# Performance work log

Hardware: AMD Instinct MI355X
Metric: run time of the kernel (lower is better)

The kernel has to match this reference:

```python
import jax, jax.numpy as jnp
import numpy as np

B, S, D = 4, 2048, 512
H, DK, DV = 8, 64, 64

def setup_inputs() -> dict:
    key = jax.random.key(0)
    ks = jax.random.split(key, 11)
    s = 0.02
    return {
        "q_in": jax.random.normal(ks[0], (B, S, D), jnp.float32),
        "k_in": jax.random.normal(ks[1], (B, S, D), jnp.float32),
        "v_in": jax.random.normal(ks[2], (B, S, D), jnp.float32),
        "Wq": jax.random.normal(ks[3], (H, D, DK), jnp.float32) * s,
        "bq": jax.random.normal(ks[4], (H, DK), jnp.float32) * s,
        "Wk": jax.random.normal(ks[5], (H, D, DK), jnp.float32) * s,
        "bk": jax.random.normal(ks[6], (H, DK), jnp.float32) * s,
        "Wv": jax.random.normal(ks[7], (H, D, DV), jnp.float32) * s,
        "bv": jax.random.normal(ks[8], (H, DV), jnp.float32) * s,
        "Wo": jax.random.normal(ks[9], (H * DV, D), jnp.float32) * s,
        "bo": jax.random.normal(ks[10], (D,), jnp.float32) * s,
    }


def reference(q_in, k_in, v_in, Wq, bq, Wk, bk, Wv, bv, Wo, bo):
    # Per-head Q/K/V projections, batched over heads (same math as the
    # original Python loop over SingleAttention heads).
    q = jnp.einsum("bsd,hdk->bhsk", q_in, Wq) + bq[None, :, None, :]   # [B,H,S,DK]
    k = jnp.einsum("bsd,hdk->bhsk", k_in, Wk) + bk[None, :, None, :]   # [B,H,S,DK]
    v = jnp.einsum("bsd,hdv->bhsv", v_in, Wv) + bv[None, :, None, :]   # [B,H,S,DV]
    scale = 1.0 / jnp.sqrt(jnp.float32(DK))
    scores = jnp.einsum("bhqk,bhsk->bhqs", q, k) * scale               # [B,H,S,S]
    attn = jax.nn.softmax(scores, axis=-1)
    out = jnp.einsum("bhqs,bhsv->bhqv", attn, v)                        # [B,H,S,DV]
    # concat heads along feature dim: [B,S,H*DV]
    concat = out.transpose(0, 2, 1, 3).reshape(B, S, H * DV)
    return concat @ Wo + bo                                             # [B,S,D]
```

## Files before the change

### kernel.cpp

```cpp
#include <hip/hip_runtime.h>
#include <hip/hip_bf16.h>

using bf16 = __hip_bfloat16;
typedef short short8  __attribute__((ext_vector_type(8)));
typedef short short4v __attribute__((ext_vector_type(4)));
typedef float float4v __attribute__((ext_vector_type(4)));
typedef float f32x16  __attribute__((ext_vector_type(16)));
typedef unsigned int uint4v __attribute__((ext_vector_type(4)));

#define MFMA_BF16   __builtin_amdgcn_mfma_f32_16x16x32_bf16
#define MFMA32_BF16 __builtin_amdgcn_mfma_f32_32x32x16_bf16

#define B_  4
#define S_  2048
#define D_  512
#define H_  8
#define DK_ 64

__device__ __forceinline__ short f2bf(float f) {
  bf16 h = __float2bfloat16(f);
  return *reinterpret_cast<short*>(&h);
}

__device__ __forceinline__ unsigned cvtpk(float lo, float hi) {
  unsigned r;
  asm("v_cvt_pk_bf16_f32 %0, %1, %2" : "=v"(r) : "v"(lo), "v"(hi));
  return r;
}

__device__ __forceinline__ void plswap(unsigned& a, unsigned& b) {
  asm("v_permlane32_swap_b32 %0, %1" : "+v"(a), "+v"(b));
}

__device__ __forceinline__ short8 mk8(unsigned v0, unsigned v1, unsigned v2,
                                      unsigned v3) {
  uint4v u;
  u[0] = v0; u[1] = v1; u[2] = v2; u[3] = v3;
  return __builtin_bit_cast(short8, u);
}

#define GLL(g, l) __builtin_amdgcn_global_load_lds(                        \
      (const __attribute__((address_space(1))) void*)(g),                  \
      (__attribute__((address_space(3))) void*)(l), 16, 0, 0)

__global__ __launch_bounds__(256)
void prep(const float* __restrict__ qin, const float* __restrict__ kin,
          const float* __restrict__ vin, short* __restrict__ Xb,
          const float* __restrict__ Wq, const float* __restrict__ Wk,
          const float* __restrict__ Wv, const float* __restrict__ Wo,
          short* __restrict__ WqT, short* __restrict__ WkT,
          short* __restrict__ WvT, short* __restrict__ WoT) {
  __shared__ float tile[64 * 65];
  const int bid = blockIdx.x, tid = threadIdx.x;
  const size_t NTOK = (size_t)B_ * S_ * D_;

  if (bid < 6144) {
    const int z = bid >> 11, blk = bid & 2047;
    const float* src = (z == 0) ? qin : (z == 1) ? kin : vin;
    short* dst = Xb + (size_t)z * NTOK;
    const size_t base = ((size_t)blk * 256 + tid) * 8;
    float4v f0 = *(const float4v*)&src[base];
    float4v f1 = *(const float4v*)&src[base + 4];
    short8 s;
#pragma unroll
    for (int j = 0; j < 4; j++) { s[j] = f2bf(f0[j]); s[j + 4] = f2bf(f1[j]); }
    *(short8*)&dst[base] = s;
    return;
  }

  const int tw = bid - 6144;
  const int mat = tw >> 6, t = tw & 63;
  const float* W = (mat == 0) ? Wq : (mat == 1) ? Wk : (mat == 2) ? Wv : Wo;
  short* T       = (mat == 0) ? WqT : (mat == 1) ? WkT : (mat == 2) ? WvT : WoT;

  size_t sbase, ss, dbase;
  if (mat < 3) {
    int hh = t >> 3, d0 = (t & 7) * 64;
    sbase = (size_t)hh * 32768 + (size_t)d0 * 64;
    ss = 64;
    dbase = (size_t)hh * 64 * 512 + d0;
  } else {
    int n0 = (t >> 3) * 64, k0 = (t & 7) * 64;
    sbase = (size_t)k0 * 512 + n0;
    ss = 512;
    dbase = (size_t)n0 * 512 + k0;
  }

  {
    int r = tid >> 2, c0 = (tid & 3) * 16;
#pragma unroll
    for (int j = 0; j < 4; j++)
      *(float4v*)&tile[r * 65 + c0 + j * 4] =
          *(const float4v*)&W[sbase + (size_t)r * ss + c0 + j * 4];
  }
  __syncthreads();
  {
    int c = tid >> 2, r0 = (tid & 3) * 16;
#pragma unroll
    for (int j = 0; j < 2; j++) {
      short8 s;
#pragma unroll
      for (int u = 0; u < 8; u++) s[u] = f2bf(tile[(r0 + j * 8 + u) * 65 + c]);
      *(short8*)&T[dbase + (size_t)c * 512 + r0 + j * 8] = s;
    }
  }
}

__device__ __forceinline__ void gemm_core2(const short* __restrict__ A,
                                           const short* __restrict__ Bt,
                                           int m0, int n0,
                                           short* As, short* Bs,
                                           float4v acc[4][4]) {
  const int tid  = threadIdx.x;
  const int lane = tid & 63, wave = tid >> 6;
  const int quad = lane >> 4, l16 = lane & 15;
  const int wm = (wave >> 1) * 64, wn = (wave & 1) * 64;

  auto stage = [&](int buf, int k0) {
#pragma unroll
    for (int i = 0; i < 4; i++) {
      int sl = wave * 256 + i * 64 + lane;
      int row = sl >> 3, cs = sl & 7;
      int gc = (cs ^ (row & 7)) << 3;
      GLL(&A[(size_t)(m0 + row) * 512 + k0 + gc],
          &As[buf * 8192 + (wave * 256 + i * 64) * 8]);
      GLL(&Bt[(size_t)(n0 + row) * 512 + k0 + gc],
          &Bs[buf * 8192 + (wave * 256 + i * 64) * 8]);
    }
  };
  auto comp = [&](int buf) {
#pragma unroll
    for (int ks = 0; ks < 64; ks += 32) {
      const int sr = (ks >> 3) + quad;
      short8 af[4], bfr[4];
#pragma unroll
      for (int mi = 0; mi < 4; mi++) {
        int row = wm + mi * 16 + l16;
        af[mi] = *(short8*)&As[buf * 8192 + row * 64 + ((sr ^ (row & 7)) << 3)];
      }
#pragma unroll
      for (int ni = 0; ni < 4; ni++) {
        int row = wn + ni * 16 + l16;
        bfr[ni] = *(short8*)&Bs[buf * 8192 + row * 64 + ((sr ^ (row & 7)) << 3)];
      }
#pragma unroll
      for (int mi = 0; mi < 4; mi++)
#pragma unroll
        for (int ni = 0; ni < 4; ni++)
          acc[mi][ni] = MFMA_BF16(af[mi], bfr[ni], acc[mi][ni], 0, 0, 0);
    }
  };

  stage(0, 0);
  asm volatile("s_waitcnt vmcnt(0)" ::: "memory");
  __syncthreads();
#pragma unroll
  for (int k0 = 0; k0 < 512; k0 += 128) {
    stage(1, k0 + 64);
    comp(0);
    asm volatile("s_waitcnt vmcnt(0)" ::: "memory");
    __syncthreads();
    if (k0 + 128 < 512) stage(0, k0 + 128);
    comp(1);
    asm volatile("s_waitcnt vmcnt(0)" ::: "memory");
    __syncthreads();
  }
}

__global__ __launch_bounds__(256, 2)
void qkv_gemm(const short* __restrict__ Xb,
              const short* __restrict__ WqT, const short* __restrict__ WkT,
              const short* __restrict__ WvT,
              const float* __restrict__ bq, const float* __restrict__ bk,
              const float* __restrict__ bv,
              short* __restrict__ Qp, short* __restrict__ Kp,
              short* __restrict__ Vt) {
  __shared__ __align__(16) short As[2 * 128 * 64];
  __shared__ __align__(16) short Bs[2 * 128 * 64];
  const int m0 = blockIdx.x * 128, n0 = blockIdx.y * 128;
  const int z = blockIdx.z;
  const size_t NTOK = (size_t)B_ * S_ * D_;
  const short* A    = Xb + (size_t)z * NTOK;
  const short* Bt   = (z == 0) ? WqT : (z == 1) ? WkT : WvT;
  const float* bias = (z == 0) ? bq  : (z == 1) ? bk  : bv;
  const float scale = (z == 0) ? 0.125f * 1.44269504088896f : 1.0f;

  float4v acc[4][4];
#pragma unroll
  for (int mi = 0; mi < 4; mi++)
#pragma unroll
    for (int ni = 0; ni < 4; ni++) acc[mi][ni] = (float4v){0.f, 0.f, 0.f, 0.f};

  gemm_core2(A, Bt, m0, n0, As, Bs, acc);

  const int lane = threadIdx.x & 63, wave = threadIdx.x >> 6;
  const int quad = lane >> 4, l16 = lane & 15;
  const int wm = (wave >> 1) * 64, wn = (wave & 1) * 64;

  if (z < 2) {
    short* out = (z == 0) ? Qp : Kp;
#pragma unroll
    for (int mi = 0; mi < 4; mi++) {
      int m = m0 + wm + mi * 16 + quad * 4;
      int b = m >> 11, s = m & 2047;
#pragma unroll
      for (int ni = 0; ni < 4; ni++) {
        int n = n0 + wn + ni * 16 + l16;
        int h = n >> 6, dk = n & 63;
        float bb = bias[n];
        size_t base = (((size_t)b * H_ + h) * S_ + s) * 64 + dk;
#pragma unroll
        for (int r = 0; r < 4; r++)
          out[base + (size_t)r * 64] = f2bf((acc[mi][ni][r] + bb) * scale);
      }
    }
  } else {
#pragma unroll
    for (int mi = 0; mi < 4; mi++) {
      int m = m0 + wm + mi * 16 + quad * 4;
      int b = m >> 11, s = m & 2047;
#pragma unroll
      for (int ni = 0; ni < 4; ni++) {
        int n = n0 + wn + ni * 16 + l16;
        int h = n >> 6, v = n & 63;
        float bb = bias[n];
        short4v pk;
#pragma unroll
        for (int r = 0; r < 4; r++) pk[r] = f2bf(acc[mi][ni][r] + bb);
        *(short4v*)&Vt[(((size_t)b * H_ + h) * 64 + v) * S_ + s] = pk;
      }
    }
  }
}

__global__ __launch_bounds__(512, 4)
void attn_kernel(const short* __restrict__ Qp, const short* __restrict__ Kp,
                 const short* __restrict__ Vt, short* __restrict__ Ao) {
  __shared__ __align__(16) short sh[32768];

  const int orig = blockIdx.y * gridDim.x + blockIdx.x;
  const int lb = (orig & 7) * 64 + (orig >> 3);
  const int qt = lb & 15, bh = lb >> 4;
  const int b = bh >> 3, h = bh & 7;

  const int tid = threadIdx.x;
  const int lane = tid & 63, wave = tid >> 6;
  const int wg = wave & 3, half = wave >> 2;
  const int l31 = lane & 31, hi = lane >> 5, s7 = l31 & 7;

  const short* Qb = Qp + (size_t)bh * S_ * 64;
  const short* Kb = Kp + (size_t)bh * S_ * 64 + (size_t)half * 1024 * 64;
  const short* Vb = Vt + (size_t)bh * 64 * S_;

  short8 qf[4];
  {
    const short* qrow = Qb + (size_t)(qt * 128 + wg * 32 + l31) * 64;
#pragma unroll
    for (int w = 0; w < 4; w++)
      qf[w] = *(const short8*)&qrow[w * 16 + hi * 8];
  }

  const int slot0 = wg * 128 + lane;
  const int kr0 = slot0 >> 3, kc0 = slot0 & 7;
  const int kr1 = kr0 + 8;
  const short* kg0 = Kb + (size_t)kr0 * 64 + ((kc0 ^ (kr0 & 7)) << 3);
  const short* kg1 = Kb + (size_t)kr1 * 64 + ((kc0 ^ (kr1 & 7)) << 3);
  const short* vg0 = Vb + (size_t)kr0 * S_ + half * 1024 + ((kc0 ^ (kr0 & 7)) << 3);
  const short* vg1 = Vb + (size_t)kr1 * S_ + half * 1024 + ((kc0 ^ (kr1 & 7)) << 3);

  short* Kbase = sh;
  short* Vbase = sh + 16384;

  f32x16 acc0, acc1;
#pragma unroll
  for (int r = 0; r < 16; r++) { acc0[r] = 0.f; acc1[r] = 0.f; }
  float ls0 = 0.f, ls1 = 0.f;

  {
    short* kd = Kbase + (half * 2) * 4096 + wg * 1024;
    short* vd = Vbase + (half * 2) * 4096 + wg * 1024;
    GLL(kg0, kd); GLL(kg1, kd + 512);
    GLL(vg0, vd); GLL(vg1, vd + 512);
  }
  __syncthreads();

  for (int t = 0; t < 16; t++) {
    const int cur = t & 1;
    if (t < 15) {
      short* kd = Kbase + (half * 2 + (cur ^ 1)) * 4096 + wg * 1024;
      short* vd = Vbase + (half * 2 + (cur ^ 1)) * 4096 + wg * 1024;
      GLL(kg0 + (size_t)(t + 1) * 4096, kd);
      GLL(kg1 + (size_t)(t + 1) * 4096, kd + 512);
      GLL(vg0 + (size_t)(t + 1) * 64, vd);
      GLL(vg1 + (size_t)(t + 1) * 64, vd + 512);
    }
    const short* kb = Kbase + (half * 2 + cur) * 4096;
    const short* vs = Vbase + (half * 2 + cur) * 4096;

#pragma unroll
    for (int kt = 0; kt < 2; kt++) {
      f32x16 sa;
#pragma unroll
      for (int r = 0; r < 16; r++) sa[r] = 0.f;
      __builtin_amdgcn_s_setprio(1);
#pragma unroll
      for (int w = 0; w < 4; w++) {
        short8 kf = *(const short8*)&kb[(kt * 32 + l31) * 64 +
                                        (((2 * w + hi) ^ s7) << 3)];
        sa = MFMA32_BF16(kf, qf[w], sa, 0, 0, 0);
      }
      __builtin_amdgcn_s_setprio(0);

      float pv[16];
#pragma unroll
      for (int r = 0; r < 16; r++) pv[r] = exp2f(sa[r]);
#pragma unroll
      for (int r = 0; r < 8; r++) { ls0 += pv[r]; ls1 += pv[r + 8]; }

      unsigned a0 = cvtpk(pv[0], pv[1]),  b0 = cvtpk(pv[4], pv[5]);
      plswap(a0, b0);
      unsigned c0 = cvtpk(pv[2], pv[3]),  d0 = cvtpk(pv[6], pv[7]);
      plswap(c0, d0);
      short8 pa0 = mk8(a0, c0, b0, d0);
      unsigned a1 = cvtpk(pv[8], pv[9]),  b1 = cvtpk(pv[12], pv[13]);
      plswap(a1, b1);
      unsigned c1 = cvtpk(pv[10], pv[11]), d1 = cvtpk(pv[14], pv[15]);
      plswap(c1, d1);
      short8 pa1 = mk8(a1, c1, b1, d1);

      __builtin_amdgcn_s_setprio(1);
      {
        const int kw0 = kt * 2, kw1 = kt * 2 + 1;
        short8 v00 = *(const short8*)&vs[l31 * 64 + (((2 * kw0 + hi) ^ s7) << 3)];
        short8 v10 = *(const short8*)&vs[(32 + l31) * 64 + (((2 * kw0 + hi) ^ s7) << 3)];
        acc0 = MFMA32_BF16(pa0, v00, acc0, 0, 0, 0);
        acc1 = MFMA32_BF16(pa0, v10, acc1, 0, 0, 0);
        short8 v01 = *(const short8*)&vs[l31 * 64 + (((2 * kw1 + hi) ^ s7) << 3)];
        short8 v11 = *(const short8*)&vs[(32 + l31) * 64 + (((2 * kw1 + hi) ^ s7) << 3)];
        acc0 = MFMA32_BF16(pa1, v01, acc0, 0, 0, 0);
        acc1 = MFMA32_BF16(pa1, v11, acc1, 0, 0, 0);
      }
      __builtin_amdgcn_s_setprio(0);
    }
    __syncthreads();
  }

  float lsum = ls0 + ls1;
  lsum += __shfl_xor(lsum, 32, 64);

  float* fsh = (float*)sh;
  if (half == 1) {
    const int base = wg * 2304 + lane * 36;
#pragma unroll
    for (int r = 0; r < 16; r += 4) {
      *(float4v*)&fsh[base + r] =
          (float4v){acc0[r], acc0[r + 1], acc0[r + 2], acc0[r + 3]};
      *(float4v*)&fsh[base + 16 + r] =
          (float4v){acc1[r], acc1[r + 1], acc1[r + 2], acc1[r + 3]};
    }
    if (lane < 32) fsh[9216 + wg * 32 + l31] = lsum;
  }
  __syncthreads();
  if (half == 1) return;

  {
    const int base = wg * 2304 + lane * 36;
#pragma unroll
    for (int r = 0; r < 16; r += 4) {
      float4v u0 = *(float4v*)&fsh[base + r];
      acc0[r] += u0[0]; acc0[r + 1] += u0[1];
      acc0[r + 2] += u0[2]; acc0[r + 3] += u0[3];
      float4v u1 = *(float4v*)&fsh[base + 16 + r];
      acc1[r] += u1[0]; acc1[r + 1] += u1[1];
      acc1[r + 2] += u1[2]; acc1[r + 3] += u1[3];
    }
    lsum += fsh[9216 + wg * 32 + l31];
  }
  float myrl = 1.0f / lsum;

  const size_t obase =
      ((size_t)b * S_ + (size_t)(qt * 128 + wg * 32)) * D_ + h * 64 + l31;
#pragma unroll
  for (int r = 0; r < 16; r++) {
    int q = (r & 3) + 8 * (r >> 2) + 4 * hi;
    float rl = __shfl(myrl, q, 64);
    Ao[obase + (size_t)q * D_]      = f2bf(acc0[r] * rl);
    Ao[obase + (size_t)q * D_ + 32] = f2bf(acc1[r] * rl);
  }
}

__global__ __launch_bounds__(256, 2)
void out_gemm(const short* __restrict__ A, const short* __restrict__ Bt,
              const float* __restrict__ bias, float* __restrict__ out) {
  __shared__ __align__(16) short As[2 * 128 * 64];
  __shared__ __align__(16) short Bs[2 * 128 * 64];
  const int m0 = blockIdx.x * 128, n0 = blockIdx.y * 128;

  float4v acc[4][4];
#pragma unroll
  for (int mi = 0; mi < 4; mi++)
#pragma unroll
    for (int ni = 0; ni < 4; ni++) acc[mi][ni] = (float4v){0.f, 0.f, 0.f, 0.f};

  gemm_core2(A, Bt, m0, n0, As, Bs, acc);

  const int lane = threadIdx.x & 63, wave = threadIdx.x >> 6;
  const int quad = lane >> 4, l16 = lane & 15;
  const int wm = (wave >> 1) * 64, wn = (wave & 1) * 64;
#pragma unroll
  for (int mi = 0; mi < 4; mi++) {
    int m = m0 + wm + mi * 16 + quad * 4;
#pragma unroll
    for (int ni = 0; ni < 4; ni++) {
      int n = n0 + wn + ni * 16 + l16;
      float bb = bias[n];
#pragma unroll
      for (int r = 0; r < 4; r++)
        out[(size_t)(m + r) * 512 + n] = acc[mi][ni][r] + bb;
    }
  }
}

extern "C" void kernel_launch(void* const* d_in, const int* in_sizes, int n_in,
                              void* d_out, int out_size, void* d_ws, size_t ws_size,
                              hipStream_t stream) {
  const float* qin = (const float*)d_in[0];
  const float* kin = (const float*)d_in[1];
  const float* vin = (const float*)d_in[2];
  const float* Wq  = (const float*)d_in[3];
  const float* bq  = (const float*)d_in[4];
  const float* Wk  = (const float*)d_in[5];
  const float* bk  = (const float*)d_in[6];
  const float* Wv  = (const float*)d_in[7];
  const float* bv  = (const float*)d_in[8];
  const float* Wo  = (const float*)d_in[9];
  const float* bo  = (const float*)d_in[10];
  float* out = (float*)d_out;
  short* ws  = (short*)d_ws;

  const size_t NTOK = (size_t)B_ * S_ * D_;
  short* Qp  = ws;
  short* Kp  = ws + NTOK;
  short* Vt  = ws + 2 * NTOK;
  short* Ao  = ws + 3 * NTOK;
  short* WqT = ws + 4 * NTOK;
  short* WkT = WqT + 512 * 512;
  short* WvT = WkT + 512 * 512;
  short* WoT = WvT + 512 * 512;
  short* Xb  = WoT + 512 * 512;

  prep<<<dim3(6400), 256, 0, stream>>>(qin, kin, vin, Xb, Wq, Wk, Wv, Wo,
                                       WqT, WkT, WvT, WoT);
  qkv_gemm<<<dim3(64, 4, 3), 256, 0, stream>>>(Xb, WqT, WkT, WvT,
                                               bq, bk, bv, Qp, Kp, Vt);
  attn_kernel<<<dim3(16, 32), 512, 0, stream>>>(Qp, Kp, Vt, Ao);
  out_gemm<<<dim3(64, 4), 256, 0, stream>>>(Ao, WoT, bo, out);
}
```

Measured before the change: 196.4 us.

## Halve GEMM K-tile into a shared A/B LDS buffer and raise occupancy

The shared GEMM core now stages 32-wide K slices of A and B into one interleaved, swizzled LDS buffer instead of two separate 64-wide buffers. This halves LDS use per block, and the QKV and output GEMM launch bounds go from 2 to 4 blocks per CU to add latency hiding. The explicit vmcnt(0) waits before each barrier are dropped, so LDS readiness after the direct global-to-LDS loads relies only on __syncthreads. The cost is twice as many loop iterations and barriers per K, plus a possible race if the barrier does not wait for those loads.

```diff
diff --git a/kernel.cpp b/kernel.cpp
--- a/kernel.cpp
+++ b/kernel.cpp
@@ -106,10 +106,10 @@
   }
 }
 
-__device__ __forceinline__ void gemm_core2(const short* __restrict__ A,
+__device__ __forceinline__ void gemm_core3(const short* __restrict__ A,
                                            const short* __restrict__ Bt,
                                            int m0, int n0,
-                                           short* As, short* Bs,
+                                           short* ABs,
                                            float4v acc[4][4]) {
   const int tid  = threadIdx.x;
   const int lane = tid & 63, wave = tid >> 6;
@@ -119,55 +119,49 @@
   auto stage = [&](int buf, int k0) {
 #pragma unroll
     for (int i = 0; i < 4; i++) {
-      int sl = wave * 256 + i * 64 + lane;
-      int row = sl >> 3, cs = sl & 7;
-      int gc = (cs ^ (row & 7)) << 3;
-      GLL(&A[(size_t)(m0 + row) * 512 + k0 + gc],
-          &As[buf * 8192 + (wave * 256 + i * 64) * 8]);
-      GLL(&Bt[(size_t)(n0 + row) * 512 + k0 + gc],
-          &Bs[buf * 8192 + (wave * 256 + i * 64) * 8]);
+      int q = (wave * 4 + i) * 64 + lane;
+      int row = q >> 3, p = q & 7;
+      int c = p ^ (row & 7);
+      const short* src = (c < 4)
+          ? &A [(size_t)(m0 + row) * 512 + k0 + c * 8]
+          : &Bt[(size_t)(n0 + row) * 512 + k0 + (c - 4) * 8];
+      GLL(src, &ABs[buf * 8192 + (wave * 4 + i) * 512]);
     }
   };
   auto comp = [&](int buf) {
-#pragma unroll
-    for (int ks = 0; ks < 64; ks += 32) {
-      const int sr = (ks >> 3) + quad;
-      short8 af[4], bfr[4];
-#pragma unroll
-      for (int mi = 0; mi < 4; mi++) {
-        int row = wm + mi * 16 + l16;
-        af[mi] = *(short8*)&As[buf * 8192 + row * 64 + ((sr ^ (row & 7)) << 3)];
-      }
-#pragma unroll
-      for (int ni = 0; ni < 4; ni++) {
-        int row = wn + ni * 16 + l16;
-        bfr[ni] = *(short8*)&Bs[buf * 8192 + row * 64 + ((sr ^ (row & 7)) << 3)];
-      }
-#pragma unroll
-      for (int mi = 0; mi < 4; mi++)
-#pragma unroll
-        for (int ni = 0; ni < 4; ni++)
-          acc[mi][ni] = MFMA_BF16(af[mi], bfr[ni], acc[mi][ni], 0, 0, 0);
-    }
+    short8 af[4], bfr[4];
+#pragma unroll
+    for (int mi = 0; mi < 4; mi++) {
+      int row = wm + mi * 16 + l16;
+      af[mi] = *(short8*)&ABs[buf * 8192 + row * 64 + ((quad ^ (row & 7)) << 3)];
+    }
+#pragma unroll
+    for (int ni = 0; ni < 4; ni++) {
+      int row = wn + ni * 16 + l16;
+      bfr[ni] = *(short8*)&ABs[buf * 8192 + row * 64 +
+                               (((4 + quad) ^ (row & 7)) << 3)];
+    }
+#pragma unroll
+    for (int mi = 0; mi < 4; mi++)
+#pragma unroll
+      for (int ni = 0; ni < 4; ni++)
+        acc[mi][ni] = MFMA_BF16(af[mi], bfr[ni], acc[mi][ni], 0, 0, 0);
   };
 
   stage(0, 0);
-  asm volatile("s_waitcnt vmcnt(0)" ::: "memory");
   __syncthreads();
 #pragma unroll
-  for (int k0 = 0; k0 < 512; k0 += 128) {
-    stage(1, k0 + 64);
+  for (int k = 0; k < 512; k += 64) {
+    stage(1, k + 32);
     comp(0);
-    asm volatile("s_waitcnt vmcnt(0)" ::: "memory");
     __syncthreads();
-    if (k0 + 128 < 512) stage(0, k0 + 128);
+    if (k + 64 < 512) stage(0, k + 64);
     comp(1);
-    asm volatile("s_waitcnt vmcnt(0)" ::: "memory");
     __syncthreads();
   }
 }
 
-__global__ __launch_bounds__(256, 2)
+__global__ __launch_bounds__(256, 4)
 void qkv_gemm(const short* __restrict__ Xb,
               const short* __restrict__ WqT, const short* __restrict__ WkT,
               const short* __restrict__ WvT,
@@ -175,8 +169,7 @@
               const float* __restrict__ bv,
               short* __restrict__ Qp, short* __restrict__ Kp,
               short* __restrict__ Vt) {
-  __shared__ __align__(16) short As[2 * 128 * 64];
-  __shared__ __align__(16) short Bs[2 * 128 * 64];
+  __shared__ __align__(16) short ABs[2 * 8192];
   const int m0 = blockIdx.x * 128, n0 = blockIdx.y * 128;
   const int z = blockIdx.z;
   const size_t NTOK = (size_t)B_ * S_ * D_;
@@ -191,7 +184,7 @@
 #pragma unroll
     for (int ni = 0; ni < 4; ni++) acc[mi][ni] = (float4v){0.f, 0.f, 0.f, 0.f};
 
-  gemm_core2(A, Bt, m0, n0, As, Bs, acc);
+  gemm_core3(A, Bt, m0, n0, ABs, acc);
 
   const int lane = threadIdx.x & 63, wave = threadIdx.x >> 6;
   const int quad = lane >> 4, l16 = lane & 15;
@@ -389,11 +382,10 @@
   }
 }
 
-__global__ __launch_bounds__(256, 2)
+__global__ __launch_bounds__(256, 4)
 void out_gemm(const short* __restrict__ A, const short* __restrict__ Bt,
               const float* __restrict__ bias, float* __restrict__ out) {
-  __shared__ __align__(16) short As[2 * 128 * 64];
-  __shared__ __align__(16) short Bs[2 * 128 * 64];
+  __shared__ __align__(16) short ABs[2 * 8192];
   const int m0 = blockIdx.x * 128, n0 = blockIdx.y * 128;
 
   float4v acc[4][4];
@@ -402,7 +394,7 @@
 #pragma unroll
     for (int ni = 0; ni < 4; ni++) acc[mi][ni] = (float4v){0.f, 0.f, 0.f, 0.f};
 
-  gemm_core2(A, Bt, m0, n0, As, Bs, acc);
+  gemm_core3(A, Bt, m0, n0, ABs, acc);
 
   const int lane = threadIdx.x & 63, wave = threadIdx.x >> 6;
   const int quad = lane >> 4, l16 = lane & 15;
```

Measured after the change: 190.3 us. 1.03x faster.
